# Optimization experiments

Measured on AMD Instinct MI355X. Metric: run time of the kernel, lower is better.

Reference implementation:

```python
import jax, jax.numpy as jnp
import numpy as np

N = 100000   # nodes
E = 1600000  # directed edges
BN_EPS = 1e-5


def setup_inputs() -> dict:
    key = jax.random.key(0)
    ks = jax.random.split(key, 16)
    x = jax.random.normal(ks[0], (N, 24), dtype=jnp.float32)
    edge_index = jax.random.randint(ks[1], (2, E), 0, N, dtype=jnp.int32)

    def glorot(k, fan_in, fan_out):
        s = jnp.sqrt(6.0 / (fan_in + fan_out)).astype(jnp.float32)
        return jax.random.uniform(k, (fan_in, fan_out), jnp.float32, -s, s)

    return {
        "x": x, "edge_index": edge_index,
        "W1": glorot(ks[2], 24, 128),  "b1": jnp.zeros((128,), jnp.float32),
        "g1": jnp.ones((128,), jnp.float32), "be1": jnp.zeros((128,), jnp.float32),
        "W2": glorot(ks[3], 128, 128), "b2": jnp.zeros((128,), jnp.float32),
        "g2": jnp.ones((128,), jnp.float32), "be2": jnp.zeros((128,), jnp.float32),
        "W3": glorot(ks[4], 128, 64),  "b3": jnp.zeros((64,), jnp.float32),
        "g3": jnp.ones((64,), jnp.float32), "be3": jnp.zeros((64,), jnp.float32),
        "W4": glorot(ks[5], 64, 2),    "b4": jnp.zeros((2,), jnp.float32),
    }


def _gcn_norm(edge_index, n):
    # add self loops, compute D^{-1/2}(A+I)D^{-1/2} edge weights (PyG gcn_norm)
    loop = jnp.arange(n, dtype=edge_index.dtype)
    src = jnp.concatenate([edge_index[0], loop])
    dst = jnp.concatenate([edge_index[1], loop])
    deg = jax.ops.segment_sum(jnp.ones_like(src, dtype=jnp.float32), dst, num_segments=n)
    dinv = jnp.where(deg > 0, jax.lax.rsqrt(deg), 0.0)
    norm = dinv[src] * dinv[dst]  # [E+N]
    return src, dst, norm


def _gcn_conv(x, W, b, src, dst, norm, n):
    h = x @ W                                # [N, F_out] GEMM first (PyG order)
    msg = h[src] * norm[:, None]             # gather + edge scale
    agg = jax.ops.segment_sum(msg, dst, num_segments=n)  # scatter-add
    return agg + b


def _bn(x, gamma, beta):
    # BatchNorm1d, training-mode statistics (biased variance), dropout omitted (eval)
    mean = jnp.mean(x, axis=0)
    var = jnp.var(x, axis=0)
    return (x - mean) * jax.lax.rsqrt(var + BN_EPS) * gamma + beta


def reference(x, edge_index, W1, b1, g1, be1, W2, b2, g2, be2,
              W3, b3, g3, be3, W4, b4):
    n = x.shape[0]
    src, dst, norm = _gcn_norm(edge_index, n)
    h = _bn(jax.nn.relu(_gcn_conv(x, W1, b1, src, dst, norm, n)), g1, be1)
    h = _bn(jax.nn.relu(_gcn_conv(h, W2, b2, src, dst, norm, n)), g2, be2)
    h = _bn(jax.nn.relu(_gcn_conv(h, W3, b3, src, dst, norm, n)), g3, be3)
    out = _gcn_conv(h, W4, b4, src, dst, norm, n)
    return jax.nn.log_softmax(out, axis=1)
```

## Files before the change

### kernel.cpp

```cpp
#include <hip/hip_runtime.h>
#include <hip/hip_fp16.h>

#define BN_EPS 1e-5f

__global__ void k_zero_i(int* __restrict__ p, int n) {
    int i = blockIdx.x * blockDim.x + threadIdx.x;
    if (i < n) p[i] = 0;
}

__global__ void k_count(const int* __restrict__ dst, int* __restrict__ cnt, int E) {
    int e = blockIdx.x * blockDim.x + threadIdx.x;
    if (e < E) atomicAdd(&cnt[dst[e]], 1);
}

__global__ void k_dinv(const int* __restrict__ cnt, float* __restrict__ dinv, int n) {
    int i = blockIdx.x * blockDim.x + threadIdx.x;
    if (i < n) dinv[i] = rsqrtf((float)(cnt[i] + 1));
}

__global__ void k_scan1(const int* __restrict__ cnt, int* __restrict__ rs,
                        int* __restrict__ bsum, int n) {
    __shared__ int sh[1024];
    const int t = threadIdx.x;
    const int gid = blockIdx.x * 1024 + t;
    int v = (gid < n) ? cnt[gid] : 0;
    sh[t] = v;
    __syncthreads();
    for (int off = 1; off < 1024; off <<= 1) {
        int u = (t >= off) ? sh[t - off] : 0;
        __syncthreads();
        sh[t] += u;
        __syncthreads();
    }
    if (gid < n) rs[gid] = sh[t] - v;
    if (t == 1023) bsum[blockIdx.x] = sh[1023];
}

__global__ void k_scan2(int* __restrict__ bsum, int nb) {
    __shared__ int sh[1024];
    const int t = threadIdx.x;
    int v = (t < nb) ? bsum[t] : 0;
    sh[t] = v;
    __syncthreads();
    for (int off = 1; off < 1024; off <<= 1) {
        int u = (t >= off) ? sh[t - off] : 0;
        __syncthreads();
        sh[t] += u;
        __syncthreads();
    }
    if (t < nb) bsum[t] = sh[t] - v;
}

__global__ void k_scan3(int* __restrict__ rs, int* __restrict__ cur,
                        const int* __restrict__ bsum, int n) {
    int i = blockIdx.x * blockDim.x + threadIdx.x;
    if (i < n) {
        int v = rs[i] + bsum[i >> 10];
        rs[i] = v;
        cur[i] = v;
    }
}

__global__ void k_fillx(const int* __restrict__ src, const int* __restrict__ dst,
                        int* __restrict__ cur, int* __restrict__ csrc,
                        int E, int nchunk) {
    const int chunk = blockIdx.x >> 3;
    const int myx = blockIdx.x & 7;
    const int per = (E + nchunk - 1) / nchunk;
    const int lo = chunk * per;
    const int hi = min(lo + per, E);
    for (int e = lo + threadIdx.x; e < hi; e += blockDim.x) {
        int d = dst[e];
        if (((d >> 7) & 7) == myx) {
            int pos = atomicAdd(&cur[d], 1);
            csrc[pos] = src[e];
        }
    }
}

__global__ void k_x2h(const float* __restrict__ x, __half* __restrict__ xh, int total4) {
    int i = blockIdx.x * blockDim.x + threadIdx.x;
    int idx = i * 4;
    if (idx < total4 * 4) {
        float4 v = *(const float4*)&x[idx];
        union { uint2 u; __half2 h[2]; } o;
        o.h[0] = __floats2half2_rn(v.x, v.y);
        o.h[1] = __floats2half2_rn(v.z, v.w);
        *(uint2*)&xh[idx] = o.u;
    }
}

__global__ void k_agg24h(const __half* __restrict__ xh, const int* __restrict__ rs,
                         const int* __restrict__ rend, const int* __restrict__ csrc,
                         const float* __restrict__ dinv, float* __restrict__ XA, int n) {
    const int g = threadIdx.x >> 3;
    const int j = threadIdx.x & 7;
    const bool act = (j < 6);
    union U { uint2 u; __half2 h[2]; };
    for (int d = blockIdx.x * 32 + g; d < n; d += gridDim.x * 32) {
        const float di = dinv[d];
        const int beg = rs[d], end = rend[d];
        float4 acc = make_float4(0.f, 0.f, 0.f, 0.f);
        if (act) {
            U u; u.u = *(const uint2*)&xh[(size_t)d * 24 + 4 * j];
            float2 f0 = __half22float2(u.h[0]), f1 = __half22float2(u.h[1]);
            acc.x = f0.x * di; acc.y = f0.y * di; acc.z = f1.x * di; acc.w = f1.y * di;
        }
        int e = beg;
        for (; e + 3 < end; e += 4) {
            int s0 = csrc[e], s1 = csrc[e + 1], s2 = csrc[e + 2], s3 = csrc[e + 3];
            float w0 = dinv[s0], w1 = dinv[s1], w2 = dinv[s2], w3 = dinv[s3];
            if (act) {
                U u0, u1, u2, u3;
                u0.u = *(const uint2*)&xh[(size_t)s0 * 24 + 4 * j];
                u1.u = *(const uint2*)&xh[(size_t)s1 * 24 + 4 * j];
                u2.u = *(const uint2*)&xh[(size_t)s2 * 24 + 4 * j];
                u3.u = *(const uint2*)&xh[(size_t)s3 * 24 + 4 * j];
                float2 a0 = __half22float2(u0.h[0]), b0 = __half22float2(u0.h[1]);
                float2 a1 = __half22float2(u1.h[0]), b1 = __half22float2(u1.h[1]);
                float2 a2 = __half22float2(u2.h[0]), b2 = __half22float2(u2.h[1]);
                float2 a3 = __half22float2(u3.h[0]), b3 = __half22float2(u3.h[1]);
                acc.x = fmaf(a0.x, w0, acc.x); acc.y = fmaf(a0.y, w0, acc.y);
                acc.z = fmaf(b0.x, w0, acc.z); acc.w = fmaf(b0.y, w0, acc.w);
                acc.x = fmaf(a1.x, w1, acc.x); acc.y = fmaf(a1.y, w1, acc.y);
                acc.z = fmaf(b1.x, w1, acc.z); acc.w = fmaf(b1.y, w1, acc.w);
                acc.x = fmaf(a2.x, w2, acc.x); acc.y = fmaf(a2.y, w2, acc.y);
                acc.z = fmaf(b2.x, w2, acc.z); acc.w = fmaf(b2.y, w2, acc.w);
                acc.x = fmaf(a3.x, w3, acc.x); acc.y = fmaf(a3.y, w3, acc.y);
                acc.z = fmaf(b3.x, w3, acc.z); acc.w = fmaf(b3.y, w3, acc.w);
            }
        }
        for (; e < end; ++e) {
            int s = csrc[e];
            float w = dinv[s];
            if (act) {
                U u; u.u = *(const uint2*)&xh[(size_t)s * 24 + 4 * j];
                float2 f0 = __half22float2(u.h[0]), f1 = __half22float2(u.h[1]);
                acc.x = fmaf(f0.x, w, acc.x); acc.y = fmaf(f0.y, w, acc.y);
                acc.z = fmaf(f1.x, w, acc.z); acc.w = fmaf(f1.y, w, acc.w);
            }
        }
        if (act) {
            acc.x *= di; acc.y *= di; acc.z *= di; acc.w *= di;
            *(float4*)&XA[(size_t)d * 24 + 4 * j] = acc;
        }
    }
}

template<int K, int F, int RT, bool AFF, bool EPI, bool CMIN>
__global__ __launch_bounds__(256) void k_gemm2(const float* __restrict__ X,
        const float* __restrict__ W, const float* __restrict__ aff,
        void* __restrict__ Ov, const float* __restrict__ b,
        float* __restrict__ sums, int n) {
    constexpr int COLG = F / 4;
    constexpr int ROWG = 256 / COLG;
    constexpr int TR = ROWG * RT;
    __shared__ float sW[K * F];
    __shared__ float sX[TR * K];
    __shared__ float sRed[2 * F];
    const int tid = threadIdx.x;
    const int tx = tid % COLG;
    const int ty = tid / COLG;

    for (int i = tid * 4; i < K * F; i += 1024)
        *(float4*)&sW[i] = *(const float4*)&W[i];

    float4 bv;
    float ls[4], lq[4];
    if constexpr (EPI) {
        bv = *(const float4*)&b[tx * 4];
        #pragma unroll
        for (int c = 0; c < 4; ++c) { ls[c] = 0.f; lq[c] = 0.f; }
    }

    const int ntiles = (n + TR - 1) / TR;
    for (int tile = blockIdx.x; tile < ntiles; tile += gridDim.x) {
        const int r0 = tile * TR;
        __syncthreads();
        for (int i = tid * 4; i < TR * K; i += 1024) {
            const int row = i / K;
            const int kk = i % K;
            float4 v;
            if (r0 + row < n) {
                if constexpr (CMIN)
                    v = *(const float4*)&X[((size_t)(kk >> 4) * n + (r0 + row)) * 16 + (kk & 15)];
                else
                    v = *(const float4*)&X[(size_t)(r0 + row) * K + kk];
                if constexpr (AFF) {
                    v.x = fmaf(v.x, aff[kk],     aff[K + kk]);
                    v.y = fmaf(v.y, aff[kk + 1], aff[K + kk + 1]);
                    v.z = fmaf(v.z, aff[kk + 2], aff[K + kk + 2]);
                    v.w = fmaf(v.w, aff[kk + 3], aff[K + kk + 3]);
                }
            } else {
                v = make_float4(0.f, 0.f, 0.f, 0.f);
            }
            *(float4*)&sX[i] = v;
        }
        __syncthreads();

        float acc[RT][4];
        #pragma unroll
        for (int r = 0; r < RT; ++r)
            #pragma unroll
            for (int c = 0; c < 4; ++c) acc[r][c] = 0.0f;

        for (int k4 = 0; k4 < K; k4 += 4) {
            float xk[RT][4];
            #pragma unroll
            for (int r = 0; r < RT; ++r) {
                float4 t = *(const float4*)&sX[(ty * RT + r) * K + k4];
                xk[r][0] = t.x; xk[r][1] = t.y; xk[r][2] = t.z; xk[r][3] = t.w;
            }
            float4 wv[4];
            #pragma unroll
            for (int kk = 0; kk < 4; ++kk)
                wv[kk] = *(const float4*)&sW[(k4 + kk) * F + tx * 4];
            #pragma unroll
            for (int kk = 0; kk < 4; ++kk)
                #pragma unroll
                for (int r = 0; r < RT; ++r) {
                    const float xr = xk[r][kk];
                    acc[r][0] = fmaf(xr, wv[kk].x, acc[r][0]);
                    acc[r][1] = fmaf(xr, wv[kk].y, acc[r][1]);
                    acc[r][2] = fmaf(xr, wv[kk].z, acc[r][2]);
                    acc[r][3] = fmaf(xr, wv[kk].w, acc[r][3]);
                }
        }

        #pragma unroll
        for (int r = 0; r < RT; ++r) {
            const int row = r0 + ty * RT + r;
            if (row < n) {
                const int col = tx * 4;
                const size_t oidx = ((size_t)(col >> 4) * n + row) * 16 + (col & 15);
                if constexpr (EPI) {
                    float4 o;
                    o.x = fmaxf(acc[r][0] + bv.x, 0.f);
                    o.y = fmaxf(acc[r][1] + bv.y, 0.f);
                    o.z = fmaxf(acc[r][2] + bv.z, 0.f);
                    o.w = fmaxf(acc[r][3] + bv.w, 0.f);
                    ls[0] += o.x; lq[0] += o.x * o.x;
                    ls[1] += o.y; lq[1] += o.y * o.y;
                    ls[2] += o.z; lq[2] += o.z * o.z;
                    ls[3] += o.w; lq[3] += o.w * o.w;
                    *(float4*)&((float*)Ov)[oidx] = o;
                } else {
                    union { float2 f2; __half2 h2[2]; } u;
                    u.h2[0] = __floats2half2_rn(acc[r][0], acc[r][1]);
                    u.h2[1] = __floats2half2_rn(acc[r][2], acc[r][3]);
                    *(float2*)&((__half*)Ov)[oidx] = u.f2;
                }
            }
        }
    }

    if constexpr (EPI) {
        __syncthreads();
        if (tid < 2 * F) sRed[tid] = 0.f;
        __syncthreads();
        #pragma unroll
        for (int c = 0; c < 4; ++c) {
            atomicAdd(&sRed[tx * 4 + c], ls[c]);
            atomicAdd(&sRed[F + tx * 4 + c], lq[c]);
        }
        __syncthreads();
        if (tid < F) {
            atomicAdd(&sums[tid], sRed[tid]);
            atomicAdd(&sums[F + tid], sRed[F + tid]);
        }
    }
}

template<int NC>
__global__ __launch_bounds__(256) void k_aggc(const __half2* __restrict__ Hc,
        const int* __restrict__ rs, const int* __restrict__ rend,
        const int* __restrict__ csrc, const float* __restrict__ dinv,
        const float* __restrict__ b, float* __restrict__ A,
        float* __restrict__ sums, int n) {
    constexpr int F = NC * 16;
    const int xcd = blockIdx.x & 7;
    const int seq = blockIdx.x >> 3;
    const int bpx = gridDim.x >> 3;
    int chunk, bindex, nper;
    if constexpr (NC == 8) { chunk = xcd; bindex = seq; nper = bpx; }
    else { chunk = xcd >> 1; bindex = seq * 2 + (xcd & 1); nper = bpx * 2; }
    const __half2* __restrict__ Hp = Hc + (size_t)chunk * n * 8;
    const int g = threadIdx.x >> 3;
    const int fl = threadIdx.x & 7;
    const int col = chunk * 16 + 2 * fl;
    const float2 bv = make_float2(b[col], b[col + 1]);
    float ls0 = 0.f, lq0 = 0.f, ls1 = 0.f, lq1 = 0.f;

    for (int d = bindex * 32 + g; d < n; d += nper * 32) {
        const int beg = rs[d], end = rend[d];
        const float di = dinv[d];
        float2 h = __half22float2(Hp[(size_t)d * 8 + fl]);
        float ax = h.x * di, ay = h.y * di;
        int j = beg;
        for (; j + 7 < end; j += 8) {
            int s[8];
            #pragma unroll
            for (int k = 0; k < 8; ++k) s[k] = csrc[j + k];
            float w[8]; __half2 hv[8];
            #pragma unroll
            for (int k = 0; k < 8; ++k) {
                w[k] = dinv[s[k]];
                hv[k] = Hp[(size_t)s[k] * 8 + fl];
            }
            #pragma unroll
            for (int k = 0; k < 8; ++k) {
                float2 f = __half22float2(hv[k]);
                ax = fmaf(f.x, w[k], ax);
                ay = fmaf(f.y, w[k], ay);
            }
        }
        for (; j + 3 < end; j += 4) {
            int s[4];
            #pragma unroll
            for (int k = 0; k < 4; ++k) s[k] = csrc[j + k];
            float w[4]; __half2 hv[4];
            #pragma unroll
            for (int k = 0; k < 4; ++k) {
                w[k] = dinv[s[k]];
                hv[k] = Hp[(size_t)s[k] * 8 + fl];
            }
            #pragma unroll
            for (int k = 0; k < 4; ++k) {
                float2 f = __half22float2(hv[k]);
                ax = fmaf(f.x, w[k], ax);
                ay = fmaf(f.y, w[k], ay);
            }
        }
        for (; j < end; ++j) {
            int s = csrc[j];
            float w = dinv[s];
            float2 f = __half22float2(Hp[(size_t)s * 8 + fl]);
            ax = fmaf(f.x, w, ax);
            ay = fmaf(f.y, w, ay);
        }
        float vx = fmaxf(fmaf(ax, di, bv.x), 0.f);
        float vy = fmaxf(fmaf(ay, di, bv.y), 0.f);
        *(float2*)&A[((size_t)chunk * n + d) * 16 + 2 * fl] = make_float2(vx, vy);
        ls0 += vx; lq0 += vx * vx;
        ls1 += vy; lq1 += vy * vy;
    }

    __shared__ float sR[32];
    if (threadIdx.x < 32) sR[threadIdx.x] = 0.f;
    __syncthreads();
    atomicAdd(&sR[2 * fl], ls0);
    atomicAdd(&sR[2 * fl + 1], ls1);
    atomicAdd(&sR[16 + 2 * fl], lq0);
    atomicAdd(&sR[16 + 2 * fl + 1], lq1);
    __syncthreads();
    if (threadIdx.x < 16) {
        atomicAdd(&sums[chunk * 16 + threadIdx.x], sR[threadIdx.x]);
        atomicAdd(&sums[F + chunk * 16 + threadIdx.x], sR[16 + threadIdx.x]);
    }
}

__global__ void k_bnprep(const float* __restrict__ sums, const float* __restrict__ g,
                         const float* __restrict__ be, float* __restrict__ aff,
                         int F, float invn) {
    int f = threadIdx.x;
    if (f < F) {
        float mean = sums[f] * invn;
        float var = sums[F + f] * invn - mean * mean;
        float a = rsqrtf(var + BN_EPS) * g[f];
        aff[f] = a;
        aff[F + f] = be[f] - mean * a;
    }
}

__global__ void k_gemm4(const float* __restrict__ X, const float* __restrict__ W,
                        const float* __restrict__ aff, float* __restrict__ H, int n) {
    int i = blockIdx.x * blockDim.x + threadIdx.x;
    if (i >= n) return;
    float a0 = 0.0f, a1 = 0.0f;
    #pragma unroll 8
    for (int k = 0; k < 64; ++k) {
        float v = X[((size_t)(k >> 4) * n + i) * 16 + (k & 15)] * aff[k] + aff[64 + k];
        a0 = fmaf(v, W[2 * k], a0);
        a1 = fmaf(v, W[2 * k + 1], a1);
    }
    H[2 * i] = a0;
    H[2 * i + 1] = a1;
}

__global__ void k_last(const float* __restrict__ H, const int* __restrict__ rs,
                       const int* __restrict__ rend, const int* __restrict__ csrc,
                       const float* __restrict__ dinv, const float* __restrict__ b,
                       float* __restrict__ out, int n) {
    int d = blockIdx.x * blockDim.x + threadIdx.x;
    if (d >= n) return;
    const float di = dinv[d];
    float a0 = H[2 * d] * di, a1 = H[2 * d + 1] * di;
    const int beg = rs[d], end = rend[d];
    for (int j = beg; j < end; ++j) {
        int s = csrc[j];
        float w = dinv[s];
        a0 = fmaf(H[2 * s], w, a0);
        a1 = fmaf(H[2 * s + 1], w, a1);
    }
    float v0 = fmaf(a0, di, b[0]);
    float v1 = fmaf(a1, di, b[1]);
    float m = fmaxf(v0, v1);
    float l = logf(expf(v0 - m) + expf(v1 - m)) + m;
    out[2 * d] = v0 - l;
    out[2 * d + 1] = v1 - l;
}

extern "C" void kernel_launch(void* const* d_in, const int* in_sizes, int n_in,
                              void* d_out, int out_size, void* d_ws, size_t ws_size,
                              hipStream_t stream) {
    const float* x   = (const float*)d_in[0];
    const int*   ei  = (const int*)d_in[1];
    const float* W1  = (const float*)d_in[2];
    const float* b1  = (const float*)d_in[3];
    const float* g1  = (const float*)d_in[4];
    const float* be1 = (const float*)d_in[5];
    const float* W2  = (const float*)d_in[6];
    const float* b2  = (const float*)d_in[7];
    const float* g2  = (const float*)d_in[8];
    const float* be2 = (const float*)d_in[9];
    const float* W3  = (const float*)d_in[10];
    const float* b3  = (const float*)d_in[11];
    const float* g3  = (const float*)d_in[12];
    const float* be3 = (const float*)d_in[13];
    const float* W4  = (const float*)d_in[14];
    const float* b4  = (const float*)d_in[15];
    float* out = (float*)d_out;

    const int N = in_sizes[0] / 24;
    const int E = in_sizes[1] / 2;
    const int* srcI = ei;
    const int* dstI = ei + E;

    int* cnt   = (int*)d_ws;
    int* rs    = cnt + N;
    int* cur   = rs + N;
    int* csrc  = cur + N;
    int* bsum  = csrc + E;
    float* dinv = (float*)(bsum + 1024);
    float* Hbase = dinv + N;
    float* A    = Hbase + (size_t)N * 128;
    float* S    = A + (size_t)N * 128;
    float* sums1 = S,        *aff1 = S + 256;
    float* sums2 = S + 512,  *aff2 = S + 768;
    float* sums3 = S + 1024, *aff3 = S + 1152;
    float*  XA    = Hbase;
    __half* Hh    = (__half*)Hbase;
    float*  LG    = Hbase;
    __half* xh    = (__half*)A;

    hipMemsetAsync(S, 0, 1280 * sizeof(float), stream);

    const int TB = 256;
    const int nb1024 = (N + 1023) / 1024;

    k_zero_i<<<(N + TB - 1) / TB, TB, 0, stream>>>(cnt, N);
    k_count<<<(E + TB - 1) / TB, TB, 0, stream>>>(dstI, cnt, E);
    k_dinv<<<(N + TB - 1) / TB, TB, 0, stream>>>(cnt, dinv, N);
    k_scan1<<<nb1024, 1024, 0, stream>>>(cnt, rs, bsum, N);
    k_scan2<<<1, 1024, 0, stream>>>(bsum, nb1024);
    k_scan3<<<(N + TB - 1) / TB, TB, 0, stream>>>(rs, cur, bsum, N);
    k_fillx<<<256 * 8, TB, 0, stream>>>(srcI, dstI, cur, csrc, E, 256);

    k_x2h<<<(N * 24 / 4 + TB - 1) / TB, TB, 0, stream>>>(x, xh, N * 24 / 4);
    k_agg24h<<<2048, 256, 0, stream>>>(xh, rs, cur, csrc, dinv, XA, N);
    k_gemm2<24, 128, 4, false, true, false><<<1024, 256, 0, stream>>>(XA, W1, nullptr, A, b1, sums1, N);
    k_bnprep<<<1, 128, 0, stream>>>(sums1, g1, be1, aff1, 128, 1.0f / (float)N);

    k_gemm2<128, 128, 4, true, false, true><<<1024, 256, 0, stream>>>(A, W2, aff1, Hh, nullptr, nullptr, N);
    k_aggc<8><<<1024, 256, 0, stream>>>((const __half2*)Hh, rs, cur, csrc, dinv, b2, A, sums2, N);
    k_bnprep<<<1, 128, 0, stream>>>(sums2, g2, be2, aff2, 128, 1.0f / (float)N);

    k_gemm2<128, 64, 2, true, false, true><<<1024, 256, 0, stream>>>(A, W3, aff2, Hh, nullptr, nullptr, N);
    k_aggc<4><<<1024, 256, 0, stream>>>((const __half2*)Hh, rs, cur, csrc, dinv, b3, A, sums3, N);
    k_bnprep<<<1, 64, 0, stream>>>(sums3, g3, be3, aff3, 64, 1.0f / (float)N);

    k_gemm4<<<(N + TB - 1) / TB, TB, 0, stream>>>(A, W4, aff3, LG, N);
    k_last<<<(N + TB - 1) / TB, TB, 0, stream>>>(LG, rs, cur, csrc, dinv, b4, out, N);
}
```

Measured before the change: 594.9 us.

## Sort nodes by degree for balanced aggregation and add nontemporal loads/stores

Adds a counting-sort pass (histogram, scan, fill) that builds a permutation of nodes ordered by in-degree, and makes all aggregation kernels iterate nodes through that permutation. The aim is for the lanes and groups of a wavefront to process nodes with similar edge counts, which reduces divergence and tail imbalance in the gather loops. It also switches CSR index reads and output stores in k_aggc to nontemporal hints and doubles the k_aggc grid size. The cost is three small extra launches, one extra indirection per node, and scattered output writes in place of sequential ones.

```diff
diff --git a/kernel.cpp b/kernel.cpp
--- a/kernel.cpp
+++ b/kernel.cpp
@@ -78,6 +78,52 @@
     }
 }
 
+__global__ void k_dhist(const int* __restrict__ cnt, int* __restrict__ hist, int n) {
+    __shared__ int lh[64];
+    const int b = blockIdx.x;
+    if (threadIdx.x < 64) lh[threadIdx.x] = 0;
+    __syncthreads();
+    const int S = (n + 63) >> 6;
+    const int lo = b * S, hi = min(lo + S, n);
+    for (int i = lo + threadIdx.x; i < hi; i += blockDim.x)
+        atomicAdd(&lh[min(cnt[i], 63)], 1);
+    __syncthreads();
+    if (threadIdx.x < 64) hist[threadIdx.x * 64 + b] = lh[threadIdx.x];
+}
+
+__global__ void k_dscan(int* __restrict__ hist) {
+    __shared__ int sh[1024];
+    const int t = threadIdx.x;
+    int v[4]; int s = 0;
+    #pragma unroll
+    for (int k = 0; k < 4; ++k) { v[k] = hist[t * 4 + k]; s += v[k]; }
+    sh[t] = s;
+    __syncthreads();
+    for (int off = 1; off < 1024; off <<= 1) {
+        int u = (t >= off) ? sh[t - off] : 0;
+        __syncthreads();
+        sh[t] += u;
+        __syncthreads();
+    }
+    int base = sh[t] - s;
+    #pragma unroll
+    for (int k = 0; k < 4; ++k) { hist[t * 4 + k] = base; base += v[k]; }
+}
+
+__global__ void k_dfill(const int* __restrict__ cnt, const int* __restrict__ hist,
+                        int* __restrict__ perm, int n) {
+    __shared__ int lcur[64];
+    const int b = blockIdx.x;
+    if (threadIdx.x < 64) lcur[threadIdx.x] = hist[threadIdx.x * 64 + b];
+    __syncthreads();
+    const int S = (n + 63) >> 6;
+    const int lo = b * S, hi = min(lo + S, n);
+    for (int i = lo + threadIdx.x; i < hi; i += blockDim.x) {
+        int pos = atomicAdd(&lcur[min(cnt[i], 63)], 1);
+        perm[pos] = i;
+    }
+}
+
 __global__ void k_x2h(const float* __restrict__ x, __half* __restrict__ xh, int total4) {
     int i = blockIdx.x * blockDim.x + threadIdx.x;
     int idx = i * 4;
@@ -92,12 +138,14 @@
 
 __global__ void k_agg24h(const __half* __restrict__ xh, const int* __restrict__ rs,
                          const int* __restrict__ rend, const int* __restrict__ csrc,
-                         const float* __restrict__ dinv, float* __restrict__ XA, int n) {
+                         const float* __restrict__ dinv, const int* __restrict__ perm,
+                         float* __restrict__ XA, int n) {
     const int g = threadIdx.x >> 3;
     const int j = threadIdx.x & 7;
     const bool act = (j < 6);
     union U { uint2 u; __half2 h[2]; };
-    for (int d = blockIdx.x * 32 + g; d < n; d += gridDim.x * 32) {
+    for (int ii = blockIdx.x * 32 + g; ii < n; ii += gridDim.x * 32) {
+        const int d = __builtin_nontemporal_load(&perm[ii]);
         const float di = dinv[d];
         const int beg = rs[d], end = rend[d];
         float4 acc = make_float4(0.f, 0.f, 0.f, 0.f);
@@ -276,8 +324,8 @@
 __global__ __launch_bounds__(256) void k_aggc(const __half2* __restrict__ Hc,
         const int* __restrict__ rs, const int* __restrict__ rend,
         const int* __restrict__ csrc, const float* __restrict__ dinv,
-        const float* __restrict__ b, float* __restrict__ A,
-        float* __restrict__ sums, int n) {
+        const int* __restrict__ perm, const float* __restrict__ b,
+        float* __restrict__ A, float* __restrict__ sums, int n) {
     constexpr int F = NC * 16;
     const int xcd = blockIdx.x & 7;
     const int seq = blockIdx.x >> 3;
@@ -292,8 +340,10 @@
     const float2 bv = make_float2(b[col], b[col + 1]);
     float ls0 = 0.f, lq0 = 0.f, ls1 = 0.f, lq1 = 0.f;
 
-    for (int d = bindex * 32 + g; d < n; d += nper * 32) {
-        const int beg = rs[d], end = rend[d];
+    for (int ii = bindex * 32 + g; ii < n; ii += nper * 32) {
+        const int d = __builtin_nontemporal_load(&perm[ii]);
+        const int beg = __builtin_nontemporal_load(&rs[d]);
+        const int end = __builtin_nontemporal_load(&rend[d]);
         const float di = dinv[d];
         float2 h = __half22float2(Hp[(size_t)d * 8 + fl]);
         float ax = h.x * di, ay = h.y * di;
@@ -301,7 +351,7 @@
         for (; j + 7 < end; j += 8) {
             int s[8];
             #pragma unroll
-            for (int k = 0; k < 8; ++k) s[k] = csrc[j + k];
+            for (int k = 0; k < 8; ++k) s[k] = __builtin_nontemporal_load(&csrc[j + k]);
             float w[8]; __half2 hv[8];
             #pragma unroll
             for (int k = 0; k < 8; ++k) {
@@ -318,7 +368,7 @@
         for (; j + 3 < end; j += 4) {
             int s[4];
             #pragma unroll
-            for (int k = 0; k < 4; ++k) s[k] = csrc[j + k];
+            for (int k = 0; k < 4; ++k) s[k] = __builtin_nontemporal_load(&csrc[j + k]);
             float w[4]; __half2 hv[4];
             #pragma unroll
             for (int k = 0; k < 4; ++k) {
@@ -333,7 +383,7 @@
             }
         }
         for (; j < end; ++j) {
-            int s = csrc[j];
+            int s = __builtin_nontemporal_load(&csrc[j]);
             float w = dinv[s];
             float2 f = __half22float2(Hp[(size_t)s * 8 + fl]);
             ax = fmaf(f.x, w, ax);
@@ -341,7 +391,10 @@
         }
         float vx = fmaxf(fmaf(ax, di, bv.x), 0.f);
         float vy = fmaxf(fmaf(ay, di, bv.y), 0.f);
-        *(float2*)&A[((size_t)chunk * n + d) * 16 + 2 * fl] = make_float2(vx, vy);
+        union { float2 f; double dd; } uo;
+        uo.f = make_float2(vx, vy);
+        __builtin_nontemporal_store(uo.dd,
+            (double*)&A[((size_t)chunk * n + d) * 16 + 2 * fl]);
         ls0 += vx; lq0 += vx * vx;
         ls1 += vy; lq1 += vy * vy;
     }
@@ -390,10 +443,11 @@
 
 __global__ void k_last(const float* __restrict__ H, const int* __restrict__ rs,
                        const int* __restrict__ rend, const int* __restrict__ csrc,
-                       const float* __restrict__ dinv, const float* __restrict__ b,
-                       float* __restrict__ out, int n) {
-    int d = blockIdx.x * blockDim.x + threadIdx.x;
-    if (d >= n) return;
+                       const float* __restrict__ dinv, const int* __restrict__ perm,
+                       const float* __restrict__ b, float* __restrict__ out, int n) {
+    int i = blockIdx.x * blockDim.x + threadIdx.x;
+    if (i >= n) return;
+    const int d = perm[i];
     const float di = dinv[d];
     float a0 = H[2 * d] * di, a1 = H[2 * d + 1] * di;
     const int beg = rs[d], end = rend[d];
@@ -442,7 +496,9 @@
     int* cur   = rs + N;
     int* csrc  = cur + N;
     int* bsum  = csrc + E;
-    float* dinv = (float*)(bsum + 1024);
+    int* perm  = bsum + 1024;
+    int* hist  = perm + N;
+    float* dinv = (float*)(hist + 4096);
     float* Hbase = dinv + N;
     float* A    = Hbase + (size_t)N * 128;
     float* S    = A + (size_t)N * 128;
@@ -466,20 +522,23 @@
     k_scan2<<<1, 1024, 0, stream>>>(bsum, nb1024);
     k_scan3<<<(N + TB - 1) / TB, TB, 0, stream>>>(rs, cur, bsum, N);
     k_fillx<<<256 * 8, TB, 0, stream>>>(srcI, dstI, cur, csrc, E, 256);
+    k_dhist<<<64, TB, 0, stream>>>(cnt, hist, N);
+    k_dscan<<<1, 1024, 0, stream>>>(hist);
+    k_dfill<<<64, TB, 0, stream>>>(cnt, hist, perm, N);
 
     k_x2h<<<(N * 24 / 4 + TB - 1) / TB, TB, 0, stream>>>(x, xh, N * 24 / 4);
-    k_agg24h<<<2048, 256, 0, stream>>>(xh, rs, cur, csrc, dinv, XA, N);
+    k_agg24h<<<2048, 256, 0, stream>>>(xh, rs, cur, csrc, dinv, perm, XA, N);
     k_gemm2<24, 128, 4, false, true, false><<<1024, 256, 0, stream>>>(XA, W1, nullptr, A, b1, sums1, N);
     k_bnprep<<<1, 128, 0, stream>>>(sums1, g1, be1, aff1, 128, 1.0f / (float)N);
 
     k_gemm2<128, 128, 4, true, false, true><<<1024, 256, 0, stream>>>(A, W2, aff1, Hh, nullptr, nullptr, N);
-    k_aggc<8><<<1024, 256, 0, stream>>>((const __half2*)Hh, rs, cur, csrc, dinv, b2, A, sums2, N);
+    k_aggc<8><<<2048, 256, 0, stream>>>((const __half2*)Hh, rs, cur, csrc, dinv, perm, b2, A, sums2, N);
     k_bnprep<<<1, 128, 0, stream>>>(sums2, g2, be2, aff2, 128, 1.0f / (float)N);
 
     k_gemm2<128, 64, 2, true, false, true><<<1024, 256, 0, stream>>>(A, W3, aff2, Hh, nullptr, nullptr, N);
-    k_aggc<4><<<1024, 256, 0, stream>>>((const __half2*)Hh, rs, cur, csrc, dinv, b3, A, sums3, N);
+    k_aggc<4><<<2048, 256, 0, stream>>>((const __half2*)Hh, rs, cur, csrc, dinv, perm, b3, A, sums3, N);
     k_bnprep<<<1, 64, 0, stream>>>(sums3, g3, be3, aff3, 64, 1.0f / (float)N);
 
     k_gemm4<<<(N + TB - 1) / TB, TB, 0, stream>>>(A, W4, aff3, LG, N);
-    k_last<<<(N + TB - 1) / TB, TB, 0, stream>>>(LG, rs, cur, csrc, dinv, b4, out, N);
-}
+    k_last<<<(N + TB - 1) / TB, TB, 0, stream>>>(LG, rs, cur, csrc, dinv, perm, b4, out, N);
+}
```

After: 807.9 us. +35.8%, slower.
